# Performance work log

Measured on AMD Instinct MI355X. Metric: run time of the kernel, lower is better.

## Reference

```python
import jax, jax.numpy as jnp
import numpy as np

# Layer widths of the fixed ClassicPINN stack: 3 -> 8x7 -> 16x3 -> 32x3 -> 16 -> 3
WIDTHS = [3, 8, 8, 8, 8, 8, 8, 8, 16, 16, 16, 32, 32, 32, 16, 3]
N_LAYERS = 15
OUT_SIZES = [1, 1, 1]
N_POINTS = 1048576


def setup_inputs() -> dict:
    key = jax.random.key(0)
    ks = jax.random.split(key, 1 + 2 * N_LAYERS)
    inp = {"coords": jax.random.normal(ks[0], (N_POINTS, WIDTHS[0]), dtype=jnp.float32)}
    # PyTorch nn.Linear default init: U(-1/sqrt(fan_in), 1/sqrt(fan_in)) for W and b
    for i in range(N_LAYERS):
        fan_in, fan_out = WIDTHS[i], WIDTHS[i + 1]
        bound = 1.0 / np.sqrt(fan_in)
        inp[f"W{i}"] = jax.random.uniform(ks[1 + 2 * i], (fan_out, fan_in), jnp.float32, -bound, bound)
        inp[f"b{i}"] = jax.random.uniform(ks[2 + 2 * i], (fan_out,), jnp.float32, -bound, bound)
    return inp


def reference(coords, W0, W1, W2, W3, W4, W5, W6, W7, W8, W9, W10, W11, W12, W13, W14,
              b0, b1, b2, b3, b4, b5, b6, b7, b8, b9, b10, b11, b12, b13, b14):
    Ws = [W0, W1, W2, W3, W4, W5, W6, W7, W8, W9, W10, W11, W12, W13, W14]
    bs = [b0, b1, b2, b3, b4, b5, b6, b7, b8, b9, b10, b11, b12, b13, b14]
    h = coords  # [N, 3]
    for i in range(N_LAYERS):
        h = h @ Ws[i].T + bs[i]
        if i < N_LAYERS - 1:  # Tanh after every layer except the last
            h = jnp.tanh(h)
    # torch.split(output, [1,1,1], dim=1)
    return (h[:, 0:1], h[:, 1:2], h[:, 2:3])
```

## Files before the change

kernel.cpp:

```cpp
#include <hip/hip_runtime.h>


#define NPTS 1048576

struct PinnParams {
    const float* W[15];
    const float* B[15];
};

__device__ __forceinline__ float fast_tanh(float x) {
    x = fminf(fmaxf(x, -9.5f), 9.5f);
    float e = __builtin_amdgcn_exp2f(x * 2.8853900817779268f);
    return 1.0f - 2.0f * __builtin_amdgcn_rcpf(e + 1.0f);
}

template <int IN, int OUT, int LAYER, bool TANH>
__device__ __forceinline__ void layer(const PinnParams& p, const float* h, float* o) {
    const float* __restrict__ W = p.W[LAYER];
    const float* __restrict__ B = p.B[LAYER];
#pragma unroll
    for (int j = 0; j < OUT; ++j) {
        float acc = B[j];
#pragma unroll
        for (int k = 0; k < IN; ++k)
            acc = fmaf(W[j * IN + k], h[k], acc);
        o[j] = TANH ? fast_tanh(acc) : acc;
    }
}

__global__ __launch_bounds__(256) void pinn_fwd(const float* __restrict__ coords,
                                                PinnParams p,
                                                float* __restrict__ out) {
    const int i = blockIdx.x * 256 + threadIdx.x;
    float h0[3];
    h0[0] = coords[3 * i + 0];
    h0[1] = coords[3 * i + 1];
    h0[2] = coords[3 * i + 2];

    float a[32], c[32];
    layer<3, 8, 0, true>(p, h0, a);
    layer<8, 8, 1, true>(p, a, c);
    layer<8, 8, 2, true>(p, c, a);
    layer<8, 8, 3, true>(p, a, c);
    layer<8, 8, 4, true>(p, c, a);
    layer<8, 8, 5, true>(p, a, c);
    layer<8, 8, 6, true>(p, c, a);
    layer<8, 16, 7, true>(p, a, c);
    layer<16, 16, 8, true>(p, c, a);
    layer<16, 16, 9, true>(p, a, c);
    layer<16, 32, 10, true>(p, c, a);
    layer<32, 32, 11, true>(p, a, c);
    layer<32, 32, 12, true>(p, c, a);
    layer<32, 16, 13, true>(p, a, c);
    layer<16, 3, 14, false>(p, c, a);

    out[i] = a[0];
    out[NPTS + i] = a[1];
    out[2 * NPTS + i] = a[2];
}

extern "C" void kernel_launch(void* const* d_in, const int* in_sizes, int n_in,
                              void* d_out, int out_size, void* d_ws, size_t ws_size,
                              hipStream_t stream) {
    const float* coords = (const float*)d_in[0];
    PinnParams p;
    for (int l = 0; l < 15; ++l) {
        p.W[l] = (const float*)d_in[1 + 2 * l];
        p.B[l] = (const float*)d_in[2 + 2 * l];
    }
    pinn_fwd<<<NPTS / 256, 256, 0, stream>>>(coords, p, (float*)d_out);
}
```

Baseline: 293.0 us.

## Process two points per thread and load weights as float4

Each thread now evaluates two points, so every weight load (now vectorized as float4) is reused across both points' accumulators. This cuts scalar weight-load instructions per FMA, and the final outputs are written as float2. It doubles the live activation registers, which may lower occupancy, and halves the grid size.

Result: no change. 291.5 us (-0.5%).

```diff
diff --git a/kernel.cpp b/kernel.cpp
--- a/kernel.cpp
+++ b/kernel.cpp
@@ -2,6 +2,7 @@
 
 
 #define NPTS 1048576
+#define P 2
 
 struct PinnParams {
     const float* W[15];
@@ -14,59 +15,93 @@
     return 1.0f - 2.0f * __builtin_amdgcn_rcpf(e + 1.0f);
 }
 
-template <int IN, int OUT, int LAYER, bool TANH>
-__device__ __forceinline__ void layer(const PinnParams& p, const float* h, float* o) {
-    const float* __restrict__ W = p.W[LAYER];
-    const float* __restrict__ B = p.B[LAYER];
+template <int IN, int OUT, bool TANH>
+__device__ __forceinline__ void layerP(const float* __restrict__ W,
+                                       const float* __restrict__ B,
+                                       const float (*h)[32], float (*o)[32]) {
+    static_assert(IN % 4 == 0, "IN must be multiple of 4");
 #pragma unroll
     for (int j = 0; j < OUT; ++j) {
-        float acc = B[j];
+        const float b = B[j];
+        float acc[P];
 #pragma unroll
-        for (int k = 0; k < IN; ++k)
-            acc = fmaf(W[j * IN + k], h[k], acc);
-        o[j] = TANH ? fast_tanh(acc) : acc;
+        for (int p = 0; p < P; ++p) acc[p] = b;
+#pragma unroll
+        for (int k = 0; k < IN; k += 4) {
+            const float4 w = *reinterpret_cast<const float4*>(W + j * IN + k);
+#pragma unroll
+            for (int p = 0; p < P; ++p) {
+                acc[p] = fmaf(w.x, h[p][k + 0], acc[p]);
+                acc[p] = fmaf(w.y, h[p][k + 1], acc[p]);
+                acc[p] = fmaf(w.z, h[p][k + 2], acc[p]);
+                acc[p] = fmaf(w.w, h[p][k + 3], acc[p]);
+            }
+        }
+#pragma unroll
+        for (int p = 0; p < P; ++p) o[p][j] = TANH ? fast_tanh(acc[p]) : acc[p];
     }
 }
 
-__global__ __launch_bounds__(256) void pinn_fwd(const float* __restrict__ coords,
-                                                PinnParams p,
-                                                float* __restrict__ out) {
-    const int i = blockIdx.x * 256 + threadIdx.x;
-    float h0[3];
-    h0[0] = coords[3 * i + 0];
-    h0[1] = coords[3 * i + 1];
-    h0[2] = coords[3 * i + 2];
+__device__ __forceinline__ void layer0(const float* __restrict__ W,
+                                       const float* __restrict__ B,
+                                       const float (*h)[32], float (*o)[32]) {
+#pragma unroll
+    for (int j = 0; j < 8; ++j) {
+        const float w0 = W[3 * j + 0], w1 = W[3 * j + 1], w2 = W[3 * j + 2];
+        const float b = B[j];
+#pragma unroll
+        for (int p = 0; p < P; ++p) {
+            float acc = fmaf(w0, h[p][0], b);
+            acc = fmaf(w1, h[p][1], acc);
+            acc = fmaf(w2, h[p][2], acc);
+            o[p][j] = fast_tanh(acc);
+        }
+    }
+}
 
-    float a[32], c[32];
-    layer<3, 8, 0, true>(p, h0, a);
-    layer<8, 8, 1, true>(p, a, c);
-    layer<8, 8, 2, true>(p, c, a);
-    layer<8, 8, 3, true>(p, a, c);
-    layer<8, 8, 4, true>(p, c, a);
-    layer<8, 8, 5, true>(p, a, c);
-    layer<8, 8, 6, true>(p, c, a);
-    layer<8, 16, 7, true>(p, a, c);
-    layer<16, 16, 8, true>(p, c, a);
-    layer<16, 16, 9, true>(p, a, c);
-    layer<16, 32, 10, true>(p, c, a);
-    layer<32, 32, 11, true>(p, a, c);
-    layer<32, 32, 12, true>(p, c, a);
-    layer<32, 16, 13, true>(p, a, c);
-    layer<16, 3, 14, false>(p, c, a);
+__global__ __launch_bounds__(256, 2) void pinn_fwd(const float* __restrict__ coords,
+                                                   PinnParams prm,
+                                                   float* __restrict__ out) {
+    const int t = blockIdx.x * 256 + threadIdx.x;
+    const int i0 = t * P;
 
-    out[i] = a[0];
-    out[NPTS + i] = a[1];
-    out[2 * NPTS + i] = a[2];
+    float a[P][32], c[P][32];
+#pragma unroll
+    for (int p = 0; p < P; ++p) {
+        a[p][0] = coords[3 * (i0 + p) + 0];
+        a[p][1] = coords[3 * (i0 + p) + 1];
+        a[p][2] = coords[3 * (i0 + p) + 2];
+    }
+
+    layer0(prm.W[0], prm.B[0], a, c);
+    layerP<8, 8, true>(prm.W[1], prm.B[1], c, a);
+    layerP<8, 8, true>(prm.W[2], prm.B[2], a, c);
+    layerP<8, 8, true>(prm.W[3], prm.B[3], c, a);
+    layerP<8, 8, true>(prm.W[4], prm.B[4], a, c);
+    layerP<8, 8, true>(prm.W[5], prm.B[5], c, a);
+    layerP<8, 8, true>(prm.W[6], prm.B[6], a, c);
+    layerP<8, 16, true>(prm.W[7], prm.B[7], c, a);
+    layerP<16, 16, true>(prm.W[8], prm.B[8], a, c);
+    layerP<16, 16, true>(prm.W[9], prm.B[9], c, a);
+    layerP<16, 32, true>(prm.W[10], prm.B[10], a, c);
+    layerP<32, 32, true>(prm.W[11], prm.B[11], c, a);
+    layerP<32, 32, true>(prm.W[12], prm.B[12], a, c);
+    layerP<32, 16, true>(prm.W[13], prm.B[13], c, a);
+    layerP<16, 3, false>(prm.W[14], prm.B[14], a, c);
+
+    *reinterpret_cast<float2*>(out + i0) = make_float2(c[0][0], c[1][0]);
+    *reinterpret_cast<float2*>(out + NPTS + i0) = make_float2(c[0][1], c[1][1]);
+    *reinterpret_cast<float2*>(out + 2 * NPTS + i0) = make_float2(c[0][2], c[1][2]);
 }
 
 extern "C" void kernel_launch(void* const* d_in, const int* in_sizes, int n_in,
                               void* d_out, int out_size, void* d_ws, size_t ws_size,
                               hipStream_t stream) {
     const float* coords = (const float*)d_in[0];
-    PinnParams p;
+    PinnParams prm;
     for (int l = 0; l < 15; ++l) {
-        p.W[l] = (const float*)d_in[1 + 2 * l];
-        p.B[l] = (const float*)d_in[2 + 2 * l];
+        prm.W[l] = (const float*)d_in[1 + 2 * l];
+        prm.B[l] = (const float*)d_in[2 + 2 * l];
     }
-    pinn_fwd<<<NPTS / 256, 256, 0, stream>>>(coords, p, (float*)d_out);
+    pinn_fwd<<<NPTS / (256 * P), 256, 0, stream>>>(coords, prm, (float*)d_out);
 }
```
